# Optimization experiments

Hardware: AMD Instinct MI355X
Metric: run time of the kernel (lower is better)

Reference implementation:

```python
import jax, jax.numpy as jnp
import numpy as np

TAU = 0.1

def setup_inputs() -> dict:
    key = jax.random.key(0)
    kZ, k1, k2 = jax.random.split(key, 3)
    N, D = 8192, 128
    scale = 1.0 / np.sqrt(D)
    return {
        "Z": jax.random.normal(kZ, (N, D), dtype=jnp.float32),
        "W1": jax.random.normal(k1, (D, D), dtype=jnp.float32) * scale,
        "b1": jnp.zeros((D,), dtype=jnp.float32),
        "W2": jax.random.normal(k2, (D, D), dtype=jnp.float32) * scale,
        "b2": jnp.zeros((D,), dtype=jnp.float32),
    }

def reference(Z, W1, b1, W2, b2):
    # DiffusivityTransform: 2-layer MLP with ReLU (torch Linear: x @ W.T + b;
    # here W1/W2 are stored already transposed as [in, out])
    t = jax.nn.relu(Z @ W1 + b1) @ W2 + b2          # [N, D]
    sim = t @ t.T                                     # [N, N]
    S = jax.nn.softmax(sim, axis=1)                   # row-stochastic [N, N]
    Z_prop = S @ Z                                    # [N, D]
    return Z + TAU * (Z_prop - Z)
```

## Files before the change

kernel.cpp:

```cpp
#include <hip/hip_runtime.h>

typedef _Float16 half_t;
typedef _Float16 hx8 __attribute__((ext_vector_type(8)));
typedef _Float16 hx4 __attribute__((ext_vector_type(4)));
typedef float fx4 __attribute__((ext_vector_type(4)));

#define LOG2E 1.44269504088896f
#define TAU 0.1f
#define NSPLIT 8

__global__ __launch_bounds__(128) void mlpz_kernel(
    const float* __restrict__ Z, const float* __restrict__ W1,
    const float* __restrict__ b1, const float* __restrict__ W2,
    const float* __restrict__ b2, half_t* __restrict__ T,
    half_t* __restrict__ Zth)
{
  __shared__ float Ztile[32*132];
  __shared__ half_t Hs[2][16*136];
  const int tid = threadIdx.x;
  const int w = tid >> 6, lane = tid & 63;
  const int q = lane >> 4, c = lane & 15;
  const int rb = blockIdx.x*32;
  const int wrow = rb + w*16;

#pragma unroll
  for (int i=0;i<8;++i) {
    int fid = i*128 + tid;
    int r = fid >> 5, c4 = (fid & 31)*4;
    *(fx4*)(&Ztile[r*132 + c4]) = *(const fx4*)(Z + (size_t)(rb + r)*128 + c4);
  }
  __syncthreads();

  {
    const int d = tid;
#pragma unroll
    for (int i=0;i<4;++i) {
      hx8 hv;
#pragma unroll
      for (int u=0;u<8;++u) hv[u] = (half_t)Ztile[(i*8 + u)*132 + d];
      *(hx8*)(Zth + (size_t)d*8192 + rb + i*8) = hv;
    }
  }

  hx8 zb[4];
#pragma unroll
  for (int ks=0;ks<4;++ks) {
    fx4 a = *(const fx4*)(&Ztile[(w*16 + c)*132 + ks*32 + q*8]);
    fx4 b = *(const fx4*)(&Ztile[(w*16 + c)*132 + ks*32 + q*8 + 4]);
#pragma unroll
    for (int u=0;u<4;++u) { zb[ks][u] = (half_t)a[u]; zb[ks][4+u] = (half_t)b[u]; }
  }

  fx4 acc[8];
#pragma unroll
  for (int mt=0;mt<8;++mt) acc[mt] = (fx4){0.f,0.f,0.f,0.f};
#pragma unroll
  for (int mt=0;mt<8;++mt)
#pragma unroll
    for (int ks=0;ks<4;++ks) {
      hx8 aw;
#pragma unroll
      for (int j=0;j<8;++j)
        aw[j] = (half_t)W1[(size_t)(ks*32 + q*8 + j)*128 + mt*16 + c];
      acc[mt] = __builtin_amdgcn_mfma_f32_16x16x32_f16(aw, zb[ks], acc[mt], 0,0,0);
    }
#pragma unroll
  for (int mt=0;mt<8;++mt) {
    fx4 bias = *(const fx4*)(b1 + mt*16 + 4*q);
    hx4 hv;
#pragma unroll
    for (int i=0;i<4;++i) {
      float h = acc[mt][i] + bias[i];
      hv[i] = (half_t)(h > 0.f ? h : 0.f);
    }
    *(hx4*)(&Hs[w][c*136 + mt*16 + 4*q]) = hv;
  }

  hx8 hb[4];
#pragma unroll
  for (int ks=0;ks<4;++ks) hb[ks] = *(const hx8*)(&Hs[w][c*136 + ks*32 + q*8]);
#pragma unroll
  for (int mt=0;mt<8;++mt) acc[mt] = (fx4){0.f,0.f,0.f,0.f};
#pragma unroll
  for (int mt=0;mt<8;++mt)
#pragma unroll
    for (int ks=0;ks<4;++ks) {
      hx8 aw;
#pragma unroll
      for (int j=0;j<8;++j)
        aw[j] = (half_t)W2[(size_t)(ks*32 + q*8 + j)*128 + mt*16 + c];
      acc[mt] = __builtin_amdgcn_mfma_f32_16x16x32_f16(aw, hb[ks], acc[mt], 0,0,0);
    }
#pragma unroll
  for (int mt=0;mt<8;++mt) {
    fx4 bias = *(const fx4*)(b2 + mt*16 + 4*q);
    hx4 tv;
#pragma unroll
    for (int i=0;i<4;++i) tv[i] = (half_t)(acc[mt][i] + bias[i]);
    *(hx4*)(T + (size_t)(wrow + c)*128 + mt*16 + 4*q) = tv;
  }
}

__global__ __launch_bounds__(256,2) void flash_kernel(
    const half_t* __restrict__ T, const half_t* __restrict__ Zt,
    half_t* __restrict__ Pacc, float* __restrict__ Pm, float* __restrict__ Pl)
{
  __shared__ half_t Tbuf[2][16*512];
  __shared__ half_t Zbuf[2][16*512];
  const int tid = threadIdx.x;
  const int w = tid >> 6, lane = tid & 63;
  const int q = lane >> 4, c = lane & 15;
  const int bx = blockIdx.x;
  const int qb = bx >> 3, kh = bx & 7;
  const int wrow = qb*128 + w*32;
  const int sw = (c & 7) * 8;

  hx8 bq[2][4];
#pragma unroll
  for (int nt=0;nt<2;++nt)
#pragma unroll
    for (int ks=0;ks<4;++ks)
      bq[nt][ks] = *(const hx8*)(T + (size_t)(wrow + nt*16 + c)*128 + ks*32 + q*8);

  fx4 oacc[8][2];
#pragma unroll
  for (int mtd=0;mtd<8;++mtd)
#pragma unroll
    for (int nt=0;nt<2;++nt) oacc[mtd][nt] = (fx4){0.f,0.f,0.f,0.f};
  float m_run[2] = {-1e30f,-1e30f};
  float l_run[2] = {0.f,0.f};

  const int kbase = kh*1024;

  auto issue_loads = [&](int kt0, int b) {
    if (w < 2) {
#pragma unroll
      for (int i=0;i<8;++i) {
        int f = w*8 + i, mt = f >> 2, ks = f & 3;
        const half_t* gp = T + (size_t)(kt0 + mt*16 + c)*128 + ks*32 + q*8;
        half_t* lp = &Tbuf[b][f*512 + lane*8];
        __builtin_amdgcn_global_load_lds(
            (const __attribute__((address_space(1))) void*)gp,
            (__attribute__((address_space(3))) void*)lp, 16, 0, 0);
      }
    } else {
#pragma unroll
      for (int i=0;i<8;++i) {
        int f2 = (w-2)*8 + i, mtd = f2 >> 1, ks2 = f2 & 1;
        const half_t* gp = Zt + (size_t)(mtd*16 + c)*8192 + kt0 + ks2*32 + q*8;
        half_t* lp = &Zbuf[b][f2*512 + lane*8];
        __builtin_amdgcn_global_load_lds(
            (const __attribute__((address_space(1))) void*)gp,
            (__attribute__((address_space(3))) void*)lp, 16, 0, 0);
      }
    }
  };

  issue_loads(kbase, 0);

  for (int t=0;t<16;++t) {
    const int cur = t & 1;
    __syncthreads();
    half_t* Tcur = Tbuf[cur];
    half_t* Zcur = Zbuf[cur];
    half_t* Psw  = &Tbuf[cur][w*2048];

    fx4 sacc[4][2];
#pragma unroll
    for (int mt=0;mt<4;++mt)
#pragma unroll
      for (int nt=0;nt<2;++nt) sacc[mt][nt] = (fx4){0.f,0.f,0.f,0.f};
#pragma unroll
    for (int ks=0;ks<4;++ks)
#pragma unroll
      for (int mt=0;mt<4;++mt) {
        hx8 ak = *(const hx8*)(&Tcur[(mt*4+ks)*512 + lane*8]);
        sacc[mt][0] = __builtin_amdgcn_mfma_f32_16x16x32_f16(ak, bq[0][ks], sacc[mt][0], 0,0,0);
        sacc[mt][1] = __builtin_amdgcn_mfma_f32_16x16x32_f16(ak, bq[1][ks], sacc[mt][1], 0,0,0);
      }

    hx4 pk[2][4];
#pragma unroll
    for (int nt=0;nt<2;++nt) {
      float mx = -1e30f;
#pragma unroll
      for (int mt=0;mt<4;++mt)
#pragma unroll
        for (int i=0;i<4;++i) mx = fmaxf(mx, sacc[mt][nt][i]);
      mx = fmaxf(mx, __shfl_xor(mx, 16, 64));
      mx = fmaxf(mx, __shfl_xor(mx, 32, 64));
      float mnew = fmaxf(m_run[nt], mx);
      float alpha = __builtin_amdgcn_exp2f((m_run[nt]-mnew)*LOG2E);
      m_run[nt] = mnew;
      float nb = mnew*LOG2E;
      float rs = 0.f;
#pragma unroll
      for (int mt=0;mt<4;++mt) {
#pragma unroll
        for (int i=0;i<4;++i) {
          float p = __builtin_amdgcn_exp2f(sacc[mt][nt][i]*LOG2E - nb);
          rs += p;
          pk[nt][mt][i] = (half_t)p;
        }
      }
      rs += __shfl_xor(rs, 16, 64);
      rs += __shfl_xor(rs, 32, 64);
      l_run[nt] = l_run[nt]*alpha + rs;
#pragma unroll
      for (int mtd=0;mtd<8;++mtd)
#pragma unroll
        for (int i=0;i<4;++i) oacc[mtd][nt][i] *= alpha;
    }

    __syncthreads();
    if (t < 15) issue_loads(kbase + (t+1)*64, cur ^ 1);

#pragma unroll
    for (int nt=0;nt<2;++nt)
#pragma unroll
      for (int mt=0;mt<4;++mt)
        *(hx4*)(&Psw[(nt*16 + c)*64 + ((mt*16 + 4*q) ^ sw)]) = pk[nt][mt];

#pragma unroll
    for (int ks2=0;ks2<2;++ks2) {
      hx8 bp0 = *(const hx8*)(&Psw[(c     )*64 + ((ks2*32 + q*8) ^ sw)]);
      hx8 bp1 = *(const hx8*)(&Psw[(16 + c)*64 + ((ks2*32 + q*8) ^ sw)]);
#pragma unroll
      for (int mtd=0;mtd<8;++mtd) {
        hx8 az = *(const hx8*)(&Zcur[(mtd*2+ks2)*512 + lane*8]);
        oacc[mtd][0] = __builtin_amdgcn_mfma_f32_16x16x32_f16(az, bp0, oacc[mtd][0], 0,0,0);
        oacc[mtd][1] = __builtin_amdgcn_mfma_f32_16x16x32_f16(az, bp1, oacc[mtd][1], 0,0,0);
      }
    }
  }

#pragma unroll
  for (int nt=0;nt<2;++nt) {
    float inv = 1.0f / l_run[nt];
    const size_t rowg = (size_t)(bx*128 + w*32 + nt*16 + c);
#pragma unroll
    for (int mtd=0;mtd<8;++mtd) {
      hx4 ov;
#pragma unroll
      for (int i=0;i<4;++i) ov[i] = (half_t)(oacc[mtd][nt][i]*inv);
      *(hx4*)(Pacc + rowg*128 + mtd*16 + 4*q) = ov;
    }
    if (q == 0) {
      Pm[rowg] = m_run[nt];
      Pl[rowg] = l_run[nt];
    }
  }
}

__global__ __launch_bounds__(256) void merge_kernel(
    const float* __restrict__ Z, const half_t* __restrict__ Pacc,
    const float* __restrict__ Pm, const float* __restrict__ Pl,
    float* __restrict__ out)
{
  const int th = blockIdx.x*256 + threadIdx.x;
  const int r = th >> 5, cg = th & 31;
  const int qb = r >> 7, rr = r & 127;
  float mk[NSPLIT], lk[NSPLIT];
  float M = -1e30f;
#pragma unroll
  for (int k=0;k<NSPLIT;++k) {
    int p = qb*NSPLIT + k;
    mk[k] = Pm[p*128 + rr];
    lk[k] = Pl[p*128 + rr];
    M = fmaxf(M, mk[k]);
  }
  float L = 0.f, wk[NSPLIT];
#pragma unroll
  for (int k=0;k<NSPLIT;++k) { wk[k] = lk[k]*__builtin_amdgcn_exp2f((mk[k]-M)*LOG2E); L += wk[k]; }
  float o0=0.f,o1=0.f,o2=0.f,o3=0.f;
#pragma unroll
  for (int k=0;k<NSPLIT;++k) {
    int p = qb*NSPLIT + k;
    hx4 v = *(const hx4*)(Pacc + ((size_t)p*128 + rr)*128 + cg*4);
    o0 += wk[k]*(float)v[0]; o1 += wk[k]*(float)v[1];
    o2 += wk[k]*(float)v[2]; o3 += wk[k]*(float)v[3];
  }
  float invL = 1.0f / L;
  fx4 zv = *(const fx4*)(Z + (size_t)r*128 + cg*4);
  fx4 res;
  res[0] = (1.f-TAU)*zv[0] + TAU*o0*invL;
  res[1] = (1.f-TAU)*zv[1] + TAU*o1*invL;
  res[2] = (1.f-TAU)*zv[2] + TAU*o2*invL;
  res[3] = (1.f-TAU)*zv[3] + TAU*o3*invL;
  *(fx4*)(out + (size_t)r*128 + cg*4) = res;
}

extern "C" void kernel_launch(void* const* d_in, const int* in_sizes, int n_in,
                              void* d_out, int out_size, void* d_ws, size_t ws_size,
                              hipStream_t stream) {
  const float* Z  = (const float*)d_in[0];
  const float* W1 = (const float*)d_in[1];
  const float* b1 = (const float*)d_in[2];
  const float* W2 = (const float*)d_in[3];
  const float* b2 = (const float*)d_in[4];
  float* out = (float*)d_out;

  char* ws = (char*)d_ws;
  const size_t NBLK = 64 * NSPLIT;
  half_t* Thi  = (half_t*)(ws);
  half_t* Zth  = (half_t*)(ws + (size_t)2*1024*1024);
  half_t* Pacc = (half_t*)(ws + (size_t)4*1024*1024);
  float*  Pm   = (float*)(ws + (size_t)4*1024*1024 + NBLK*128*128*2);
  float*  Pl   = Pm + NBLK*128;

  hipLaunchKernelGGL(mlpz_kernel,  dim3(256),  dim3(128), 0, stream, Z, W1, b1, W2, b2, Thi, Zth);
  hipLaunchKernelGGL(flash_kernel, dim3(NBLK), dim3(256), 0, stream, Thi, Zth, Pacc, Pm, Pl);
  hipLaunchKernelGGL(merge_kernel, dim3(1024), dim3(256), 0, stream, Z, Pacc, Pm, Pl, out);
}
```

Baseline: 129.6 us.

## Halve flash query tile and read Z operand directly from global memory

The flash kernel now has each wave own 16 query rows instead of 32, making the block tile 64 rows and doubling the grid to 1024 blocks. The shared Z staging buffer is removed, and the Z^T fragments for the P·Z MFMA are read straight from global memory (relying on cache). This halves the shared-memory footprint and the per-thread accumulators, which should raise occupancy. In exchange, each key tile of T is loaded twice as often across blocks, Z reads are no longer overlapped through the async LDS pipeline, and the Pacc row indexing is remapped so the merge layout stays the same.

```diff
diff --git a/kernel.cpp b/kernel.cpp
--- a/kernel.cpp
+++ b/kernel.cpp
@@ -106,53 +106,36 @@
     half_t* __restrict__ Pacc, float* __restrict__ Pm, float* __restrict__ Pl)
 {
   __shared__ half_t Tbuf[2][16*512];
-  __shared__ half_t Zbuf[2][16*512];
   const int tid = threadIdx.x;
   const int w = tid >> 6, lane = tid & 63;
   const int q = lane >> 4, c = lane & 15;
   const int bx = blockIdx.x;
   const int qb = bx >> 3, kh = bx & 7;
-  const int wrow = qb*128 + w*32;
+  const int wrow = qb*64 + w*16;
   const int sw = (c & 7) * 8;
 
-  hx8 bq[2][4];
-#pragma unroll
-  for (int nt=0;nt<2;++nt)
-#pragma unroll
-    for (int ks=0;ks<4;++ks)
-      bq[nt][ks] = *(const hx8*)(T + (size_t)(wrow + nt*16 + c)*128 + ks*32 + q*8);
-
-  fx4 oacc[8][2];
-#pragma unroll
-  for (int mtd=0;mtd<8;++mtd)
-#pragma unroll
-    for (int nt=0;nt<2;++nt) oacc[mtd][nt] = (fx4){0.f,0.f,0.f,0.f};
-  float m_run[2] = {-1e30f,-1e30f};
-  float l_run[2] = {0.f,0.f};
+  hx8 bq[4];
+#pragma unroll
+  for (int ks=0;ks<4;++ks)
+    bq[ks] = *(const hx8*)(T + (size_t)(wrow + c)*128 + ks*32 + q*8);
+
+  fx4 oacc[8];
+#pragma unroll
+  for (int mtd=0;mtd<8;++mtd) oacc[mtd] = (fx4){0.f,0.f,0.f,0.f};
+  float m_run = -1e30f;
+  float l_run = 0.f;
 
   const int kbase = kh*1024;
 
   auto issue_loads = [&](int kt0, int b) {
-    if (w < 2) {
-#pragma unroll
-      for (int i=0;i<8;++i) {
-        int f = w*8 + i, mt = f >> 2, ks = f & 3;
-        const half_t* gp = T + (size_t)(kt0 + mt*16 + c)*128 + ks*32 + q*8;
-        half_t* lp = &Tbuf[b][f*512 + lane*8];
-        __builtin_amdgcn_global_load_lds(
-            (const __attribute__((address_space(1))) void*)gp,
-            (__attribute__((address_space(3))) void*)lp, 16, 0, 0);
-      }
-    } else {
-#pragma unroll
-      for (int i=0;i<8;++i) {
-        int f2 = (w-2)*8 + i, mtd = f2 >> 1, ks2 = f2 & 1;
-        const half_t* gp = Zt + (size_t)(mtd*16 + c)*8192 + kt0 + ks2*32 + q*8;
-        half_t* lp = &Zbuf[b][f2*512 + lane*8];
-        __builtin_amdgcn_global_load_lds(
-            (const __attribute__((address_space(1))) void*)gp,
-            (__attribute__((address_space(3))) void*)lp, 16, 0, 0);
-      }
+#pragma unroll
+    for (int i=0;i<4;++i) {
+      int f = w*4 + i, mt = f >> 2, ks = f & 3;
+      const half_t* gp = T + (size_t)(kt0 + mt*16 + c)*128 + ks*32 + q*8;
+      half_t* lp = &Tbuf[b][f*512 + lane*8];
+      __builtin_amdgcn_global_load_lds(
+          (const __attribute__((address_space(1))) void*)gp,
+          (__attribute__((address_space(3))) void*)lp, 16, 0, 0);
     }
   };
 
@@ -162,93 +145,79 @@
     const int cur = t & 1;
     __syncthreads();
     half_t* Tcur = Tbuf[cur];
-    half_t* Zcur = Zbuf[cur];
-    half_t* Psw  = &Tbuf[cur][w*2048];
-
-    fx4 sacc[4][2];
-#pragma unroll
-    for (int mt=0;mt<4;++mt)
-#pragma unroll
-      for (int nt=0;nt<2;++nt) sacc[mt][nt] = (fx4){0.f,0.f,0.f,0.f};
+    half_t* Psw  = &Tbuf[cur][w*1024];
+
+    fx4 sacc[4];
+#pragma unroll
+    for (int mt=0;mt<4;++mt) sacc[mt] = (fx4){0.f,0.f,0.f,0.f};
 #pragma unroll
     for (int ks=0;ks<4;++ks)
 #pragma unroll
       for (int mt=0;mt<4;++mt) {
         hx8 ak = *(const hx8*)(&Tcur[(mt*4+ks)*512 + lane*8]);
-        sacc[mt][0] = __builtin_amdgcn_mfma_f32_16x16x32_f16(ak, bq[0][ks], sacc[mt][0], 0,0,0);
-        sacc[mt][1] = __builtin_amdgcn_mfma_f32_16x16x32_f16(ak, bq[1][ks], sacc[mt][1], 0,0,0);
+        sacc[mt] = __builtin_amdgcn_mfma_f32_16x16x32_f16(ak, bq[ks], sacc[mt], 0,0,0);
       }
 
-    hx4 pk[2][4];
-#pragma unroll
-    for (int nt=0;nt<2;++nt) {
-      float mx = -1e30f;
-#pragma unroll
-      for (int mt=0;mt<4;++mt)
-#pragma unroll
-        for (int i=0;i<4;++i) mx = fmaxf(mx, sacc[mt][nt][i]);
-      mx = fmaxf(mx, __shfl_xor(mx, 16, 64));
-      mx = fmaxf(mx, __shfl_xor(mx, 32, 64));
-      float mnew = fmaxf(m_run[nt], mx);
-      float alpha = __builtin_amdgcn_exp2f((m_run[nt]-mnew)*LOG2E);
-      m_run[nt] = mnew;
-      float nb = mnew*LOG2E;
-      float rs = 0.f;
-#pragma unroll
-      for (int mt=0;mt<4;++mt) {
-#pragma unroll
-        for (int i=0;i<4;++i) {
-          float p = __builtin_amdgcn_exp2f(sacc[mt][nt][i]*LOG2E - nb);
-          rs += p;
-          pk[nt][mt][i] = (half_t)p;
-        }
+    float mx = -1e30f;
+#pragma unroll
+    for (int mt=0;mt<4;++mt)
+#pragma unroll
+      for (int i=0;i<4;++i) mx = fmaxf(mx, sacc[mt][i]);
+    mx = fmaxf(mx, __shfl_xor(mx, 16, 64));
+    mx = fmaxf(mx, __shfl_xor(mx, 32, 64));
+    float mnew = fmaxf(m_run, mx);
+    float alpha = __builtin_amdgcn_exp2f((m_run - mnew)*LOG2E);
+    m_run = mnew;
+    float nb = mnew*LOG2E;
+    float rs = 0.f;
+    hx4 pk[4];
+#pragma unroll
+    for (int mt=0;mt<4;++mt)
+#pragma unroll
+      for (int i=0;i<4;++i) {
+        float p = __builtin_amdgcn_exp2f(sacc[mt][i]*LOG2E - nb);
+        rs += p;
+        pk[mt][i] = (half_t)p;
       }
-      rs += __shfl_xor(rs, 16, 64);
-      rs += __shfl_xor(rs, 32, 64);
-      l_run[nt] = l_run[nt]*alpha + rs;
-#pragma unroll
-      for (int mtd=0;mtd<8;++mtd)
-#pragma unroll
-        for (int i=0;i<4;++i) oacc[mtd][nt][i] *= alpha;
-    }
+    rs += __shfl_xor(rs, 16, 64);
+    rs += __shfl_xor(rs, 32, 64);
+    l_run = l_run*alpha + rs;
+#pragma unroll
+    for (int mtd=0;mtd<8;++mtd)
+#pragma unroll
+      for (int i=0;i<4;++i) oacc[mtd][i] *= alpha;
 
     __syncthreads();
     if (t < 15) issue_loads(kbase + (t+1)*64, cur ^ 1);
 
 #pragma unroll
-    for (int nt=0;nt<2;++nt)
-#pragma unroll
-      for (int mt=0;mt<4;++mt)
-        *(hx4*)(&Psw[(nt*16 + c)*64 + ((mt*16 + 4*q) ^ sw)]) = pk[nt][mt];
-
+    for (int mt=0;mt<4;++mt)
+      *(hx4*)(&Psw[c*64 + ((mt*16 + 4*q) ^ sw)]) = pk[mt];
+
+    const half_t* zcol = Zt + (size_t)c*8192 + kbase + t*64 + q*8;
 #pragma unroll
     for (int ks2=0;ks2<2;++ks2) {
-      hx8 bp0 = *(const hx8*)(&Psw[(c     )*64 + ((ks2*32 + q*8) ^ sw)]);
-      hx8 bp1 = *(const hx8*)(&Psw[(16 + c)*64 + ((ks2*32 + q*8) ^ sw)]);
+      hx8 bp = *(const hx8*)(&Psw[c*64 + ((ks2*32 + q*8) ^ sw)]);
 #pragma unroll
       for (int mtd=0;mtd<8;++mtd) {
-        hx8 az = *(const hx8*)(&Zcur[(mtd*2+ks2)*512 + lane*8]);
-        oacc[mtd][0] = __builtin_amdgcn_mfma_f32_16x16x32_f16(az, bp0, oacc[mtd][0], 0,0,0);
-        oacc[mtd][1] = __builtin_amdgcn_mfma_f32_16x16x32_f16(az, bp1, oacc[mtd][1], 0,0,0);
+        hx8 az = *(const hx8*)(zcol + (size_t)mtd*16*8192 + ks2*32);
+        oacc[mtd] = __builtin_amdgcn_mfma_f32_16x16x32_f16(az, bp, oacc[mtd], 0,0,0);
       }
     }
   }
 
-#pragma unroll
-  for (int nt=0;nt<2;++nt) {
-    float inv = 1.0f / l_run[nt];
-    const size_t rowg = (size_t)(bx*128 + w*32 + nt*16 + c);
-#pragma unroll
-    for (int mtd=0;mtd<8;++mtd) {
-      hx4 ov;
-#pragma unroll
-      for (int i=0;i<4;++i) ov[i] = (half_t)(oacc[mtd][nt][i]*inv);
-      *(hx4*)(Pacc + rowg*128 + mtd*16 + 4*q) = ov;
-    }
-    if (q == 0) {
-      Pm[rowg] = m_run[nt];
-      Pl[rowg] = l_run[nt];
-    }
+  float inv = 1.0f / l_run;
+  const size_t prow = (size_t)(((qb >> 1)*8 + kh)*128 + (qb & 1)*64 + w*16 + c);
+#pragma unroll
+  for (int mtd=0;mtd<8;++mtd) {
+    hx4 ov;
+#pragma unroll
+    for (int i=0;i<4;++i) ov[i] = (half_t)(oacc[mtd][i]*inv);
+    *(hx4*)(Pacc + prow*128 + mtd*16 + 4*q) = ov;
+  }
+  if (q == 0) {
+    Pm[prow] = m_run;
+    Pl[prow] = l_run;
   }
 }
 
@@ -309,6 +278,6 @@
   float*  Pl   = Pm + NBLK*128;
 
   hipLaunchKernelGGL(mlpz_kernel,  dim3(256),  dim3(128), 0, stream, Z, W1, b1, W2, b2, Thi, Zth);
-  hipLaunchKernelGGL(flash_kernel, dim3(NBLK), dim3(256), 0, stream, Thi, Zth, Pacc, Pm, Pl);
+  hipLaunchKernelGGL(flash_kernel, dim3(128*NSPLIT), dim3(256), 0, stream, Thi, Zth, Pacc, Pm, Pl);
   hipLaunchKernelGGL(merge_kernel, dim3(1024), dim3(256), 0, stream, Z, Pacc, Pm, Pl, out);
 }
```

Result: slower. 227.1 us (+75.3%).

## Split MLP across more blocks and halve flash key-tile size

Applied to the files above, without the earlier changes.

The MLP kernel now processes 16 rows per block with 256 threads. Each wave computes two output column tiles of the shared row tile, with a block-wide sync between the two layers. The flash kernel's key tile drops from 64 to 32 keys per iteration, so it runs twice as many iterations with half the shared memory. The smaller footprint is meant to raise occupancy and parallelism. In exchange the flash kernel pays more per-iteration overhead (syncs, softmax rescaling of the output accumulators) and issues smaller MFMA batches between barriers.

```diff
diff --git a/kernel.cpp b/kernel.cpp
--- a/kernel.cpp
+++ b/kernel.cpp
@@ -9,95 +9,87 @@
 #define TAU 0.1f
 #define NSPLIT 8
 
-__global__ __launch_bounds__(128) void mlpz_kernel(
+__global__ __launch_bounds__(256) void mlpz_kernel(
     const float* __restrict__ Z, const float* __restrict__ W1,
     const float* __restrict__ b1, const float* __restrict__ W2,
     const float* __restrict__ b2, half_t* __restrict__ T,
     half_t* __restrict__ Zth)
 {
-  __shared__ float Ztile[32*132];
-  __shared__ half_t Hs[2][16*136];
+  __shared__ float Ztile[16*132];
+  __shared__ half_t Hs[16*136];
   const int tid = threadIdx.x;
   const int w = tid >> 6, lane = tid & 63;
   const int q = lane >> 4, c = lane & 15;
-  const int rb = blockIdx.x*32;
-  const int wrow = rb + w*16;
-
-#pragma unroll
-  for (int i=0;i<8;++i) {
-    int fid = i*128 + tid;
+  const int rb = blockIdx.x*16;
+
+#pragma unroll
+  for (int i=0;i<2;++i) {
+    int fid = i*256 + tid;
     int r = fid >> 5, c4 = (fid & 31)*4;
     *(fx4*)(&Ztile[r*132 + c4]) = *(const fx4*)(Z + (size_t)(rb + r)*128 + c4);
   }
   __syncthreads();
 
   {
-    const int d = tid;
-#pragma unroll
-    for (int i=0;i<4;++i) {
-      hx8 hv;
-#pragma unroll
-      for (int u=0;u<8;++u) hv[u] = (half_t)Ztile[(i*8 + u)*132 + d];
-      *(hx8*)(Zth + (size_t)d*8192 + rb + i*8) = hv;
-    }
+    const int d = tid & 127, h = tid >> 7;
+    hx8 hv;
+#pragma unroll
+    for (int u=0;u<8;++u) hv[u] = (half_t)Ztile[(h*8 + u)*132 + d];
+    *(hx8*)(Zth + (size_t)d*8192 + rb + h*8) = hv;
   }
 
   hx8 zb[4];
 #pragma unroll
   for (int ks=0;ks<4;++ks) {
-    fx4 a = *(const fx4*)(&Ztile[(w*16 + c)*132 + ks*32 + q*8]);
-    fx4 b = *(const fx4*)(&Ztile[(w*16 + c)*132 + ks*32 + q*8 + 4]);
+    fx4 a = *(const fx4*)(&Ztile[c*132 + ks*32 + q*8]);
+    fx4 b = *(const fx4*)(&Ztile[c*132 + ks*32 + q*8 + 4]);
 #pragma unroll
     for (int u=0;u<4;++u) { zb[ks][u] = (half_t)a[u]; zb[ks][4+u] = (half_t)b[u]; }
   }
 
-  fx4 acc[8];
-#pragma unroll
-  for (int mt=0;mt<8;++mt) acc[mt] = (fx4){0.f,0.f,0.f,0.f};
-#pragma unroll
-  for (int mt=0;mt<8;++mt)
+#pragma unroll
+  for (int m2=0;m2<2;++m2) {
+    const int mt = w*2 + m2;
+    fx4 acc = (fx4){0.f,0.f,0.f,0.f};
 #pragma unroll
     for (int ks=0;ks<4;++ks) {
       hx8 aw;
 #pragma unroll
       for (int j=0;j<8;++j)
         aw[j] = (half_t)W1[(size_t)(ks*32 + q*8 + j)*128 + mt*16 + c];
-      acc[mt] = __builtin_amdgcn_mfma_f32_16x16x32_f16(aw, zb[ks], acc[mt], 0,0,0);
-    }
-#pragma unroll
-  for (int mt=0;mt<8;++mt) {
+      acc = __builtin_amdgcn_mfma_f32_16x16x32_f16(aw, zb[ks], acc, 0,0,0);
+    }
     fx4 bias = *(const fx4*)(b1 + mt*16 + 4*q);
     hx4 hv;
 #pragma unroll
     for (int i=0;i<4;++i) {
-      float h = acc[mt][i] + bias[i];
+      float h = acc[i] + bias[i];
       hv[i] = (half_t)(h > 0.f ? h : 0.f);
     }
-    *(hx4*)(&Hs[w][c*136 + mt*16 + 4*q]) = hv;
-  }
+    *(hx4*)(&Hs[c*136 + mt*16 + 4*q]) = hv;
+  }
+  __syncthreads();
 
   hx8 hb[4];
 #pragma unroll
-  for (int ks=0;ks<4;++ks) hb[ks] = *(const hx8*)(&Hs[w][c*136 + ks*32 + q*8]);
-#pragma unroll
-  for (int mt=0;mt<8;++mt) acc[mt] = (fx4){0.f,0.f,0.f,0.f};
-#pragma unroll
-  for (int mt=0;mt<8;++mt)
+  for (int ks=0;ks<4;++ks) hb[ks] = *(const hx8*)(&Hs[c*136 + ks*32 + q*8]);
+#pragma unroll
+  for (int m2=0;m2<2;++m2) {
+    const int mt = w*2 + m2;
+    fx4 acc = (fx4){0.f,0.f,0.f,0.f};
 #pragma unroll
     for (int ks=0;ks<4;++ks) {
       hx8 aw;
 #pragma unroll
       for (int j=0;j<8;++j)
         aw[j] = (half_t)W2[(size_t)(ks*32 + q*8 + j)*128 + mt*16 + c];
-      acc[mt] = __builtin_amdgcn_mfma_f32_16x16x32_f16(aw, hb[ks], acc[mt], 0,0,0);
-    }
-#pragma unroll
-  for (int mt=0;mt<8;++mt) {
+      acc = __builtin_amdgcn_mfma_f32_16x16x32_f16(aw, hb[ks], acc, 0,0,0);
+    }
     fx4 bias = *(const fx4*)(b2 + mt*16 + 4*q);
     hx4 tv;
 #pragma unroll
-    for (int i=0;i<4;++i) tv[i] = (half_t)(acc[mt][i] + bias[i]);
-    *(hx4*)(T + (size_t)(wrow + c)*128 + mt*16 + 4*q) = tv;
+    for (int i=0;i<4;++i) tv[i] = (half_t)(acc[i] + bias[i]);
+    *(hx4*)(T + (size_t)(rb + c)*128 + mt*16 + 4*q) = tv;
   }
 }
 
@@ -105,15 +97,15 @@
     const half_t* __restrict__ T, const half_t* __restrict__ Zt,
     half_t* __restrict__ Pacc, float* __restrict__ Pm, float* __restrict__ Pl)
 {
-  __shared__ half_t Tbuf[2][16*512];
-  __shared__ half_t Zbuf[2][16*512];
+  __shared__ half_t Tbuf[2][8*512];
+  __shared__ half_t Zbuf[2][8*512];
   const int tid = threadIdx.x;
   const int w = tid >> 6, lane = tid & 63;
   const int q = lane >> 4, c = lane & 15;
   const int bx = blockIdx.x;
   const int qb = bx >> 3, kh = bx & 7;
   const int wrow = qb*128 + w*32;
-  const int sw = (c & 7) * 8;
+  const int sw = (c & 3) * 8;
 
   hx8 bq[2][4];
 #pragma unroll
@@ -135,8 +127,8 @@
   auto issue_loads = [&](int kt0, int b) {
     if (w < 2) {
 #pragma unroll
-      for (int i=0;i<8;++i) {
-        int f = w*8 + i, mt = f >> 2, ks = f & 3;
+      for (int i=0;i<4;++i) {
+        int f = w*4 + i, mt = f >> 2, ks = f & 3;
         const half_t* gp = T + (size_t)(kt0 + mt*16 + c)*128 + ks*32 + q*8;
         half_t* lp = &Tbuf[b][f*512 + lane*8];
         __builtin_amdgcn_global_load_lds(
@@ -145,9 +137,9 @@
       }
     } else {
 #pragma unroll
-      for (int i=0;i<8;++i) {
-        int f2 = (w-2)*8 + i, mtd = f2 >> 1, ks2 = f2 & 1;
-        const half_t* gp = Zt + (size_t)(mtd*16 + c)*8192 + kt0 + ks2*32 + q*8;
+      for (int i=0;i<4;++i) {
+        int f2 = (w-2)*4 + i;
+        const half_t* gp = Zt + (size_t)(f2*16 + c)*8192 + kt0 + q*8;
         half_t* lp = &Zbuf[b][f2*512 + lane*8];
         __builtin_amdgcn_global_load_lds(
             (const __attribute__((address_space(1))) void*)gp,
@@ -158,33 +150,33 @@
 
   issue_loads(kbase, 0);
 
-  for (int t=0;t<16;++t) {
+  for (int t=0;t<32;++t) {
     const int cur = t & 1;
     __syncthreads();
     half_t* Tcur = Tbuf[cur];
     half_t* Zcur = Zbuf[cur];
-    half_t* Psw  = &Tbuf[cur][w*2048];
-
-    fx4 sacc[4][2];
-#pragma unroll
-    for (int mt=0;mt<4;++mt)
+    half_t* Psw  = &Tbuf[cur][w*1024];
+
+    fx4 sacc[2][2];
+#pragma unroll
+    for (int mt=0;mt<2;++mt)
 #pragma unroll
       for (int nt=0;nt<2;++nt) sacc[mt][nt] = (fx4){0.f,0.f,0.f,0.f};
 #pragma unroll
     for (int ks=0;ks<4;++ks)
 #pragma unroll
-      for (int mt=0;mt<4;++mt) {
+      for (int mt=0;mt<2;++mt) {
         hx8 ak = *(const hx8*)(&Tcur[(mt*4+ks)*512 + lane*8]);
         sacc[mt][0] = __builtin_amdgcn_mfma_f32_16x16x32_f16(ak, bq[0][ks], sacc[mt][0], 0,0,0);
         sacc[mt][1] = __builtin_amdgcn_mfma_f32_16x16x32_f16(ak, bq[1][ks], sacc[mt][1], 0,0,0);
       }
 
-    hx4 pk[2][4];
+    hx4 pk[2][2];
 #pragma unroll
     for (int nt=0;nt<2;++nt) {
       float mx = -1e30f;
 #pragma unroll
-      for (int mt=0;mt<4;++mt)
+      for (int mt=0;mt<2;++mt)
 #pragma unroll
         for (int i=0;i<4;++i) mx = fmaxf(mx, sacc[mt][nt][i]);
       mx = fmaxf(mx, __shfl_xor(mx, 16, 64));
@@ -195,7 +187,7 @@
       float nb = mnew*LOG2E;
       float rs = 0.f;
 #pragma unroll
-      for (int mt=0;mt<4;++mt) {
+      for (int mt=0;mt<2;++mt) {
 #pragma unroll
         for (int i=0;i<4;++i) {
           float p = __builtin_amdgcn_exp2f(sacc[mt][nt][i]*LOG2E - nb);
@@ -213,21 +205,20 @@
     }
 
     __syncthreads();
-    if (t < 15) issue_loads(kbase + (t+1)*64, cur ^ 1);
+    if (t < 31) issue_loads(kbase + (t+1)*32, cur ^ 1);
 
 #pragma unroll
     for (int nt=0;nt<2;++nt)
 #pragma unroll
-      for (int mt=0;mt<4;++mt)
-        *(hx4*)(&Psw[(nt*16 + c)*64 + ((mt*16 + 4*q) ^ sw)]) = pk[nt][mt];
-
-#pragma unroll
-    for (int ks2=0;ks2<2;++ks2) {
-      hx8 bp0 = *(const hx8*)(&Psw[(c     )*64 + ((ks2*32 + q*8) ^ sw)]);
-      hx8 bp1 = *(const hx8*)(&Psw[(16 + c)*64 + ((ks2*32 + q*8) ^ sw)]);
+      for (int mt=0;mt<2;++mt)
+        *(hx4*)(&Psw[(nt*16 + c)*32 + ((mt*16 + 4*q) ^ sw)]) = pk[nt][mt];
+
+    {
+      hx8 bp0 = *(const hx8*)(&Psw[(c     )*32 + ((q*8) ^ sw)]);
+      hx8 bp1 = *(const hx8*)(&Psw[(16 + c)*32 + ((q*8) ^ sw)]);
 #pragma unroll
       for (int mtd=0;mtd<8;++mtd) {
-        hx8 az = *(const hx8*)(&Zcur[(mtd*2+ks2)*512 + lane*8]);
+        hx8 az = *(const hx8*)(&Zcur[mtd*512 + lane*8]);
         oacc[mtd][0] = __builtin_amdgcn_mfma_f32_16x16x32_f16(az, bp0, oacc[mtd][0], 0,0,0);
         oacc[mtd][1] = __builtin_amdgcn_mfma_f32_16x16x32_f16(az, bp1, oacc[mtd][1], 0,0,0);
       }
@@ -308,7 +299,7 @@
   float*  Pm   = (float*)(ws + (size_t)4*1024*1024 + NBLK*128*128*2);
   float*  Pl   = Pm + NBLK*128;
 
-  hipLaunchKernelGGL(mlpz_kernel,  dim3(256),  dim3(128), 0, stream, Z, W1, b1, W2, b2, Thi, Zth);
+  hipLaunchKernelGGL(mlpz_kernel,  dim3(512),  dim3(256), 0, stream, Z, W1, b1, W2, b2, Thi, Zth);
   hipLaunchKernelGGL(flash_kernel, dim3(NBLK), dim3(256), 0, stream, Thi, Zth, Pacc, Pm, Pl);
   hipLaunchKernelGGL(merge_kernel, dim3(1024), dim3(256), 0, stream, Z, Pacc, Pm, Pl, out);
 }
```

Result: slower. 138.9 us (+7.2%).
